# Kernel optimization log

Hardware: AMD Instinct MI355X
Metric: run time of the kernel (lower is better)

## Reference

```python
import jax, jax.numpy as jnp
import numpy as np

B, N, C, IC = 8, 4096, 1024, 256
EPS = 1e-5


def setup_inputs() -> dict:
    key = jax.random.key(0)
    ks = jax.random.split(key, 10)
    s = 0.02  # keep activations well-scaled
    return {
        "v": jax.random.normal(ks[0], (B, N, C), jnp.float32),
        "g_w": jax.random.normal(ks[1], (IC, C), jnp.float32) * s,
        "g_b": jax.random.normal(ks[2], (IC,), jnp.float32) * s,
        "theta_w": jax.random.normal(ks[3], (IC, C), jnp.float32) * s,
        "theta_b": jax.random.normal(ks[4], (IC,), jnp.float32) * s,
        "phi_w": jax.random.normal(ks[5], (IC, C), jnp.float32) * s,
        "phi_b": jax.random.normal(ks[6], (IC,), jnp.float32) * s,
        "W_w": jax.random.normal(ks[7], (C, IC), jnp.float32) * s,
        "W_b": jax.random.normal(ks[8], (C,), jnp.float32) * s,
        "bn_gamma": jnp.ones((C,), jnp.float32),
        "bn_beta": jnp.zeros((C,), jnp.float32),
    }


def reference(v, g_w, g_b, theta_w, theta_b, phi_w, phi_b, W_w, W_b, bn_gamma, bn_beta):
    # v: (B, N, C). All Conv1d(k=1) == per-token matmul.
    g_v = jnp.einsum("bnc,ic->bni", v, g_w) + g_b          # (B, N, IC)
    theta_v = jnp.einsum("bnc,ic->bni", v, theta_w) + theta_b
    phi_v = jnp.einsum("bnc,ic->bni", v, phi_w) + phi_b
    n = v.shape[1]
    # Affinity: R = theta @ phi^T, normalized by N (no softmax)
    R = jnp.einsum("bni,bmi->bnm", theta_v, phi_v) / n      # (B, N, N)
    y = jnp.einsum("bnm,bmi->bni", R, g_v)                  # (B, N, IC)
    W_y = jnp.einsum("bni,ci->bnc", y, W_w) + W_b           # (B, N, C)
    # BatchNorm1d training mode: per-channel stats over (B, N), biased var
    mean = jnp.mean(W_y, axis=(0, 1))
    var = jnp.var(W_y, axis=(0, 1))
    W_y = (W_y - mean) * jax.lax.rsqrt(var + EPS) * bn_gamma + bn_beta
    return W_y + v                                          # residual, (B, N, C)
```

## Files before the change

### kernel.cpp

```cpp
#include <hip/hip_runtime.h>
#include <hip/hip_bf16.h>
#include <stdint.h>


using bf16 = __hip_bfloat16;
typedef __attribute__((ext_vector_type(8))) short short8;
typedef __attribute__((ext_vector_type(4))) float f32x4;
typedef __attribute__((ext_vector_type(4))) short short4v;

#define DEVI static __device__ __forceinline__

DEVI float bf2f(unsigned short u) {
  union { unsigned int i; float f; } x; x.i = ((unsigned int)u) << 16; return x.f;
}
DEVI unsigned short f2bf(float f) {
  __hip_bfloat16 h = __float2bfloat16(f);
  return *reinterpret_cast<unsigned short*>(&h);
}

DEVI void gld16(const void* g, void* l) {
  __builtin_amdgcn_global_load_lds((__attribute__((address_space(1))) void*)g,
                                   (__attribute__((address_space(3))) void*)l,
                                   16, 0, 0);
}

DEVI void mfma_loop(const bf16* A, int ldA, const bf16* B, int ldB,
                    int kiters, bf16* lds_a, bf16* lds_b, f32x4 acc[4][4])
{
  const int tid = threadIdx.x;
  const int lane = tid & 63;
  const int w = tid >> 6;
  const int wr = w >> 1, wc = w & 1;
  const int srow = w * 32 + (lane >> 2);
  const int scol = (lane & 3) * 8;
  const bf16* ga0 = A + (size_t)srow * ldA + scol;
  const bf16* ga1 = A + (size_t)(srow + 16) * ldA + scol;
  const bf16* gb0 = B + (size_t)srow * ldB + scol;
  const bf16* gb1 = B + (size_t)(srow + 16) * ldB + scol;
  bf16* la0 = lds_a + w * 1024 + lane * 8;
  bf16* la1 = la0 + 512;
  bf16* lb0 = lds_b + w * 1024 + lane * 8;
  bf16* lb1 = lb0 + 512;
  const int frow = lane & 15;
  const int fk = (lane >> 4) * 8;
  const bf16* ra = lds_a + (wr * 64 + frow) * 32 + fk;
  const bf16* rb = lds_b + (wc * 64 + frow) * 32 + fk;
  for (int it = 0; it < kiters; ++it) {
    gld16(ga0, la0); gld16(ga1, la1);
    gld16(gb0, lb0); gld16(gb1, lb1);
    ga0 += 32; ga1 += 32; gb0 += 32; gb1 += 32;
    __syncthreads();
    short8 af[4], bfr[4];
#pragma unroll
    for (int i = 0; i < 4; ++i) af[i] = *(const short8*)(ra + i * 512);
#pragma unroll
    for (int j = 0; j < 4; ++j) bfr[j] = *(const short8*)(rb + j * 512);
#pragma unroll
    for (int i = 0; i < 4; ++i)
#pragma unroll
      for (int j = 0; j < 4; ++j)
        acc[i][j] = __builtin_amdgcn_mfma_f32_16x16x32_bf16(af[i], bfr[j], acc[i][j], 0, 0, 0);
    __syncthreads();
  }
}

#define ACC_INIT(acc)                                   \
  _Pragma("unroll") for (int i = 0; i < 4; ++i)         \
  _Pragma("unroll") for (int j = 0; j < 4; ++j)         \
      acc[i][j] = (f32x4){0.f, 0.f, 0.f, 0.f};

__global__ __launch_bounds__(256) void k_cast(const float* __restrict__ in, bf16* __restrict__ out)
{
  const size_t idx = ((size_t)blockIdx.x * 256 + threadIdx.x) * 8;
  float4 a = *(const float4*)(in + idx);
  float4 b = *(const float4*)(in + idx + 4);
  short8 o;
  o[0] = (short)f2bf(a.x); o[1] = (short)f2bf(a.y);
  o[2] = (short)f2bf(a.z); o[3] = (short)f2bf(a.w);
  o[4] = (short)f2bf(b.x); o[5] = (short)f2bf(b.y);
  o[6] = (short)f2bf(b.z); o[7] = (short)f2bf(b.w);
  *(short8*)(out + idx) = o;
}

__global__ __launch_bounds__(256) void k_proj(
    const bf16* __restrict__ vbf,
    const bf16* __restrict__ w_th, const float* __restrict__ b_th,
    const bf16* __restrict__ w_ph, const float* __restrict__ b_ph,
    const bf16* __restrict__ w_g,  const float* __restrict__ b_g,
    bf16* __restrict__ theta, bf16* __restrict__ phiT, bf16* __restrict__ gT)
{
  __shared__ __align__(16) char smem[34048];
  bf16* lds_a = (bf16*)smem;
  bf16* lds_b = (bf16*)(smem + 8192);
  unsigned short* lds_t = (unsigned short*)smem;

  const int tt = blockIdx.x;
  const int yy = blockIdx.y;
  const int proj = yy >> 1;
  const int icb = (yy & 1) * 128;
  const bf16* wsel = (proj == 0) ? w_th : ((proj == 1) ? w_ph : w_g);
  const float* bsel = (proj == 0) ? b_th : ((proj == 1) ? b_ph : b_g);

  const size_t t0 = (size_t)tt * 128;
  f32x4 acc[4][4];
  ACC_INIT(acc);
  mfma_loop(vbf + t0 * 1024, 1024, wsel + (size_t)icb * 1024, 1024, 32, lds_a, lds_b, acc);

  const int tid = threadIdx.x, lane = tid & 63, w = tid >> 6;
  const int wr = w >> 1, wc = w & 1, quad = lane >> 4, l15 = lane & 15;
  float biasv[4];
#pragma unroll
  for (int j = 0; j < 4; ++j) biasv[j] = bsel[icb + wc * 64 + j * 16 + l15];

  if (proj == 0) {
#pragma unroll
    for (int i = 0; i < 4; ++i)
#pragma unroll
      for (int j = 0; j < 4; ++j)
#pragma unroll
        for (int r = 0; r < 4; ++r) {
          int m = wr * 64 + i * 16 + quad * 4 + r;
          int n = wc * 64 + j * 16 + l15;
          theta[(t0 + m) * 256 + icb + n] = __float2bfloat16(acc[i][j][r] + biasv[j]);
        }
  } else {
#pragma unroll
    for (int i = 0; i < 4; ++i)
#pragma unroll
      for (int j = 0; j < 4; ++j)
#pragma unroll
        for (int r = 0; r < 4; ++r) {
          int m = wr * 64 + i * 16 + quad * 4 + r;
          int n = wc * 64 + j * 16 + l15;
          lds_t[m * 133 + n] = f2bf(acc[i][j][r] + biasv[j]);
        }
    __syncthreads();
    bf16* outT = (proj == 1) ? phiT : gT;
    const int bb = (int)(t0 >> 12);
    const int n0 = (int)(t0 & 4095);
    const int tg = tid & 7;
    const int ch0 = tid >> 3;
#pragma unroll
    for (int half = 0; half < 2; ++half)
#pragma unroll
      for (int cc = 0; cc < 4; ++cc) {
        int ch = ch0 + cc * 32;
        int tok0 = half * 64 + tg * 8;
        short8 pk;
#pragma unroll
        for (int r = 0; r < 8; ++r) pk[r] = (short)lds_t[(tok0 + r) * 133 + ch];
        *(short8*)(outT + ((size_t)(bb * 256 + icb + ch)) * 4096 + n0 + tok0) = pk;
      }
  }
}

__global__ __launch_bounds__(256) void k_affin(
    const bf16* __restrict__ phiT, const bf16* __restrict__ gT, float* __restrict__ M)
{
  __shared__ __align__(16) char smem[16384];
  bf16* lds_a = (bf16*)smem;
  bf16* lds_b = (bf16*)(smem + 8192);
  const int kc = blockIdx.x;
  const int jt = blockIdx.y >> 1;
  const int it2 = blockIdx.y & 1;
  const int bb = blockIdx.z;
  f32x4 acc[4][4];
  ACC_INIT(acc);
  const bf16* A = phiT + ((size_t)bb * 256 + jt * 128) * 4096 + kc * 512;
  const bf16* B = gT   + ((size_t)bb * 256 + it2 * 128) * 4096 + kc * 512;
  mfma_loop(A, 4096, B, 4096, 16, lds_a, lds_b, acc);
  const int tid = threadIdx.x, lane = tid & 63, w = tid >> 6;
  const int wr = w >> 1, wc = w & 1, quad = lane >> 4, l15 = lane & 15;
  float* Mb = M + (size_t)bb * 65536;
#pragma unroll
  for (int i = 0; i < 4; ++i)
#pragma unroll
    for (int j = 0; j < 4; ++j)
#pragma unroll
      for (int r = 0; r < 4; ++r) {
        int m = wr * 64 + i * 16 + quad * 4 + r;
        int n = wc * 64 + j * 16 + l15;
        atomicAdd(&Mb[(size_t)(jt * 128 + m) * 256 + it2 * 128 + n], acc[i][j][r]);
      }
}

__global__ __launch_bounds__(256) void k_mconv(const float* __restrict__ M, bf16* __restrict__ Mbf)
{
  int i = blockIdx.x * 256 + threadIdx.x;
  Mbf[i] = __float2bfloat16(M[i] * (1.0f / 4096.0f));
}

__global__ __launch_bounds__(256) void k_pt(
    const bf16* __restrict__ Ww, const bf16* __restrict__ Mbf, bf16* __restrict__ PT)
{
  __shared__ __align__(16) char smem[16384];
  bf16* lds_a = (bf16*)smem;
  bf16* lds_b = (bf16*)(smem + 8192);
  const int ct = blockIdx.x;
  const int jt = blockIdx.y;
  const int bb = blockIdx.z;
  f32x4 acc[4][4];
  ACC_INIT(acc);
  mfma_loop(Ww + (size_t)ct * 128 * 256, 256,
            Mbf + ((size_t)bb * 256 + jt * 128) * 256, 256, 8, lds_a, lds_b, acc);
  const int tid = threadIdx.x, lane = tid & 63, w = tid >> 6;
  const int wr = w >> 1, wc = w & 1, quad = lane >> 4, l15 = lane & 15;
#pragma unroll
  for (int i = 0; i < 4; ++i)
#pragma unroll
    for (int j = 0; j < 4; ++j)
#pragma unroll
      for (int r = 0; r < 4; ++r) {
        int m = wr * 64 + i * 16 + quad * 4 + r;
        int n = wc * 64 + j * 16 + l15;
        PT[((size_t)bb * 1024 + ct * 128 + m) * 256 + jt * 128 + n] = __float2bfloat16(acc[i][j][r]);
      }
}

__global__ __launch_bounds__(256) void k_wy(
    const bf16* __restrict__ theta, const bf16* __restrict__ PT, bf16* __restrict__ Wy)
{
  __shared__ __align__(16) char smem[16384];
  bf16* lds_a = (bf16*)smem;
  bf16* lds_b = (bf16*)(smem + 8192);
  const size_t t0 = (size_t)blockIdx.x * 128;
  const int ct = blockIdx.y;
  const int bb = (int)(t0 >> 12);
  f32x4 acc[4][4];
  ACC_INIT(acc);
  mfma_loop(theta + t0 * 256, 256,
            PT + ((size_t)bb * 1024 + ct * 128) * 256, 256, 8, lds_a, lds_b, acc);
  const int tid = threadIdx.x, lane = tid & 63, w = tid >> 6;
  const int wr = w >> 1, wc = w & 1, quad = lane >> 4, l15 = lane & 15;
#pragma unroll
  for (int i = 0; i < 4; ++i)
#pragma unroll
    for (int j = 0; j < 4; ++j)
#pragma unroll
      for (int r = 0; r < 4; ++r) {
        int m = wr * 64 + i * 16 + quad * 4 + r;
        int n = wc * 64 + j * 16 + l15;
        Wy[(t0 + m) * 1024 + ct * 128 + n] = __float2bfloat16(acc[i][j][r]);
      }
}

__global__ __launch_bounds__(256) void k_stats(const bf16* __restrict__ Wy,
                                               float* __restrict__ sums, float* __restrict__ sumsq)
{
  const int t0 = blockIdx.x * 128;
  const int c0 = threadIdx.x * 4;
  float s[4] = {0.f, 0.f, 0.f, 0.f}, q[4] = {0.f, 0.f, 0.f, 0.f};
  for (int r = 0; r < 128; ++r) {
    short4v u = *(const short4v*)(Wy + (size_t)(t0 + r) * 1024 + c0);
#pragma unroll
    for (int k = 0; k < 4; ++k) {
      float f = bf2f((unsigned short)u[k]);
      s[k] += f; q[k] += f * f;
    }
  }
#pragma unroll
  for (int k = 0; k < 4; ++k) {
    atomicAdd(&sums[c0 + k], s[k]);
    atomicAdd(&sumsq[c0 + k], q[k]);
  }
}

__global__ void k_norm(const float* __restrict__ sums, const float* __restrict__ sumsq,
                       const float* __restrict__ gamma, const float* __restrict__ beta,
                       float* __restrict__ scale, float* __restrict__ shift)
{
  int c = blockIdx.x * 256 + threadIdx.x;
  float mean = sums[c] * (1.0f / 32768.0f);
  float var = sumsq[c] * (1.0f / 32768.0f) - mean * mean;
  float sc = gamma[c] * rsqrtf(var + 1e-5f);
  scale[c] = sc;
  shift[c] = beta[c] - mean * sc;
}

__global__ __launch_bounds__(256) void k_out(const bf16* __restrict__ Wy, const float* __restrict__ v,
                                             const float* __restrict__ scale, const float* __restrict__ shift,
                                             float* __restrict__ out)
{
  const size_t idx = ((size_t)blockIdx.x * 256 + threadIdx.x) * 4;
  const int c = (int)(idx & 1023);
  short4v wv = *(const short4v*)(Wy + idx);
  float4 vv = *(const float4*)(v + idx);
  float4 o;
  o.x = bf2f((unsigned short)wv[0]) * scale[c + 0] + shift[c + 0] + vv.x;
  o.y = bf2f((unsigned short)wv[1]) * scale[c + 1] + shift[c + 1] + vv.y;
  o.z = bf2f((unsigned short)wv[2]) * scale[c + 2] + shift[c + 2] + vv.z;
  o.w = bf2f((unsigned short)wv[3]) * scale[c + 3] + shift[c + 3] + vv.w;
  *(float4*)(out + idx) = o;
}

extern "C" void kernel_launch(void* const* d_in, const int* in_sizes, int n_in,
                              void* d_out, int out_size, void* d_ws, size_t ws_size,
                              hipStream_t stream)
{
  (void)in_sizes; (void)n_in; (void)out_size; (void)ws_size;
  const float* v    = (const float*)d_in[0];
  const float* g_w  = (const float*)d_in[1];
  const float* g_b  = (const float*)d_in[2];
  const float* th_w = (const float*)d_in[3];
  const float* th_b = (const float*)d_in[4];
  const float* ph_w = (const float*)d_in[5];
  const float* ph_b = (const float*)d_in[6];
  const float* W_w  = (const float*)d_in[7];
  const float* gamma = (const float*)d_in[9];
  const float* beta  = (const float*)d_in[10];
  float* out = (float*)d_out;

  char* ws = (char*)d_ws;
  bf16* vbf  = (bf16*)ws;
  bf16* Wy   = (bf16*)ws;
  ws += (size_t)32768 * 1024 * 2;
  bf16* theta = (bf16*)ws;  ws += (size_t)32768 * 256 * 2;
  bf16* phiT  = (bf16*)ws;  ws += (size_t)32768 * 256 * 2;
  bf16* gT    = (bf16*)ws;  ws += (size_t)32768 * 256 * 2;
  float* M    = (float*)ws; ws += (size_t)8 * 65536 * 4;
  bf16* Mbf   = (bf16*)ws;  ws += (size_t)8 * 65536 * 2;
  bf16* PT    = (bf16*)ws;  ws += (size_t)8 * 1024 * 256 * 2;
  bf16* thwb  = (bf16*)ws;  ws += (size_t)256 * 1024 * 2;
  bf16* phwb  = (bf16*)ws;  ws += (size_t)256 * 1024 * 2;
  bf16* gwb   = (bf16*)ws;  ws += (size_t)256 * 1024 * 2;
  bf16* Wwb   = (bf16*)ws;  ws += (size_t)1024 * 256 * 2;
  float* sums = (float*)ws; ws += 4096;
  float* sumsq= (float*)ws; ws += 4096;
  float* scale= (float*)ws; ws += 4096;
  float* shift= (float*)ws; ws += 4096;

  hipMemsetAsync(M, 0, (size_t)8 * 65536 * 4, stream);
  hipMemsetAsync(sums, 0, 8192, stream);

  k_cast <<<16384, 256, 0, stream>>>(v, vbf);
  k_cast <<<128, 256, 0, stream>>>(th_w, thwb);
  k_cast <<<128, 256, 0, stream>>>(ph_w, phwb);
  k_cast <<<128, 256, 0, stream>>>(g_w, gwb);
  k_cast <<<128, 256, 0, stream>>>(W_w, Wwb);

  k_proj <<<dim3(256, 6), 256, 0, stream>>>(vbf, thwb, th_b, phwb, ph_b, gwb, g_b, theta, phiT, gT);
  k_affin<<<dim3(8, 4, 8), 256, 0, stream>>>(phiT, gT, M);
  k_mconv<<<2048, 256, 0, stream>>>(M, Mbf);
  k_pt   <<<dim3(8, 2, 8), 256, 0, stream>>>(Wwb, Mbf, PT);
  k_wy   <<<dim3(256, 8), 256, 0, stream>>>(theta, PT, Wy);
  k_stats<<<256, 256, 0, stream>>>(Wy, sums, sumsq);
  k_norm <<<4, 256, 0, stream>>>(sums, sumsq, gamma, beta, scale, shift);
  k_out  <<<32768, 256, 0, stream>>>(Wy, v, scale, shift, out);
}
```

Before: 470.7 us.

## Fuse v cast into projection GEMM and BN stats into Wy epilogue

```diff
diff --git a/kernel.cpp b/kernel.cpp
--- a/kernel.cpp
+++ b/kernel.cpp
@@ -22,6 +22,15 @@
   __builtin_amdgcn_global_load_lds((__attribute__((address_space(1))) void*)g,
                                    (__attribute__((address_space(3))) void*)l,
                                    16, 0, 0);
+}
+
+DEVI short8 cvt8(float4 a, float4 b) {
+  short8 o;
+  o[0] = (short)f2bf(a.x); o[1] = (short)f2bf(a.y);
+  o[2] = (short)f2bf(a.z); o[3] = (short)f2bf(a.w);
+  o[4] = (short)f2bf(b.x); o[5] = (short)f2bf(b.y);
+  o[6] = (short)f2bf(b.z); o[7] = (short)f2bf(b.w);
+  return o;
 }
 
 DEVI void mfma_loop(const bf16* A, int ldA, const bf16* B, int ldB,
@@ -64,26 +73,77 @@
   }
 }
 
+DEVI void mfma_loop_f32a(const float* A, int ldA, const bf16* B, int ldB,
+                         int kiters, bf16* lds_a, bf16* lds_b, f32x4 acc[4][4])
+{
+  const int tid = threadIdx.x;
+  const int lane = tid & 63;
+  const int w = tid >> 6;
+  const int wr = w >> 1, wc = w & 1;
+  const int srow = w * 32 + (lane >> 2);
+  const int scol = (lane & 3) * 8;
+  const float* ga0 = A + (size_t)srow * ldA + scol;
+  const float* ga1 = A + (size_t)(srow + 16) * ldA + scol;
+  const bf16* gb0 = B + (size_t)srow * ldB + scol;
+  const bf16* gb1 = B + (size_t)(srow + 16) * ldB + scol;
+  bf16* la0 = lds_a + w * 1024 + lane * 8;
+  bf16* la1 = la0 + 512;
+  bf16* lb0 = lds_b + w * 1024 + lane * 8;
+  bf16* lb1 = lb0 + 512;
+  const int frow = lane & 15;
+  const int fk = (lane >> 4) * 8;
+  const bf16* ra = lds_a + (wr * 64 + frow) * 32 + fk;
+  const bf16* rb = lds_b + (wc * 64 + frow) * 32 + fk;
+  for (int it = 0; it < kiters; ++it) {
+    gld16(gb0, lb0); gld16(gb1, lb1);
+    float4 a00 = *(const float4*)ga0;
+    float4 a01 = *(const float4*)(ga0 + 4);
+    float4 a10 = *(const float4*)ga1;
+    float4 a11 = *(const float4*)(ga1 + 4);
+    *(short8*)la0 = cvt8(a00, a01);
+    *(short8*)la1 = cvt8(a10, a11);
+    ga0 += 32; ga1 += 32; gb0 += 32; gb1 += 32;
+    __syncthreads();
+    short8 af[4], bfr[4];
+#pragma unroll
+    for (int i = 0; i < 4; ++i) af[i] = *(const short8*)(ra + i * 512);
+#pragma unroll
+    for (int j = 0; j < 4; ++j) bfr[j] = *(const short8*)(rb + j * 512);
+#pragma unroll
+    for (int i = 0; i < 4; ++i)
+#pragma unroll
+      for (int j = 0; j < 4; ++j)
+        acc[i][j] = __builtin_amdgcn_mfma_f32_16x16x32_bf16(af[i], bfr[j], acc[i][j], 0, 0, 0);
+    __syncthreads();
+  }
+}
+
 #define ACC_INIT(acc)                                   \
   _Pragma("unroll") for (int i = 0; i < 4; ++i)         \
   _Pragma("unroll") for (int j = 0; j < 4; ++j)         \
       acc[i][j] = (f32x4){0.f, 0.f, 0.f, 0.f};
 
-__global__ __launch_bounds__(256) void k_cast(const float* __restrict__ in, bf16* __restrict__ out)
-{
+__global__ __launch_bounds__(256) void k_castw(
+    const float* __restrict__ s0, const float* __restrict__ s1,
+    const float* __restrict__ s2, const float* __restrict__ s3,
+    bf16* __restrict__ d0, bf16* __restrict__ d1,
+    bf16* __restrict__ d2, bf16* __restrict__ d3)
+{
+  const float* in; bf16* out;
+  switch (blockIdx.y) {
+    case 0:  in = s0; out = d0; break;
+    case 1:  in = s1; out = d1; break;
+    case 2:  in = s2; out = d2; break;
+    default: in = s3; out = d3; break;
+  }
   const size_t idx = ((size_t)blockIdx.x * 256 + threadIdx.x) * 8;
   float4 a = *(const float4*)(in + idx);
   float4 b = *(const float4*)(in + idx + 4);
-  short8 o;
-  o[0] = (short)f2bf(a.x); o[1] = (short)f2bf(a.y);
-  o[2] = (short)f2bf(a.z); o[3] = (short)f2bf(a.w);
-  o[4] = (short)f2bf(b.x); o[5] = (short)f2bf(b.y);
-  o[6] = (short)f2bf(b.z); o[7] = (short)f2bf(b.w);
-  *(short8*)(out + idx) = o;
+  *(short8*)(out + idx) = cvt8(a, b);
 }
 
 __global__ __launch_bounds__(256) void k_proj(
-    const bf16* __restrict__ vbf,
+    const float* __restrict__ v,
     const bf16* __restrict__ w_th, const float* __restrict__ b_th,
     const bf16* __restrict__ w_ph, const float* __restrict__ b_ph,
     const bf16* __restrict__ w_g,  const float* __restrict__ b_g,
@@ -104,7 +164,7 @@
   const size_t t0 = (size_t)tt * 128;
   f32x4 acc[4][4];
   ACC_INIT(acc);
-  mfma_loop(vbf + t0 * 1024, 1024, wsel + (size_t)icb * 1024, 1024, 32, lds_a, lds_b, acc);
+  mfma_loop_f32a(v + t0 * 1024, 1024, wsel + (size_t)icb * 1024, 1024, 32, lds_a, lds_b, acc);
 
   const int tid = threadIdx.x, lane = tid & 63, w = tid >> 6;
   const int wr = w >> 1, wc = w & 1, quad = lane >> 4, l15 = lane & 15;
@@ -218,7 +278,8 @@
 }
 
 __global__ __launch_bounds__(256) void k_wy(
-    const bf16* __restrict__ theta, const bf16* __restrict__ PT, bf16* __restrict__ Wy)
+    const bf16* __restrict__ theta, const bf16* __restrict__ PT, bf16* __restrict__ Wy,
+    float* __restrict__ sums, float* __restrict__ sumsq)
 {
   __shared__ __align__(16) char smem[16384];
   bf16* lds_a = (bf16*)smem;
@@ -232,6 +293,7 @@
             PT + ((size_t)bb * 1024 + ct * 128) * 256, 256, 8, lds_a, lds_b, acc);
   const int tid = threadIdx.x, lane = tid & 63, w = tid >> 6;
   const int wr = w >> 1, wc = w & 1, quad = lane >> 4, l15 = lane & 15;
+  float ps[4] = {0.f, 0.f, 0.f, 0.f}, pq[4] = {0.f, 0.f, 0.f, 0.f};
 #pragma unroll
   for (int i = 0; i < 4; ++i)
 #pragma unroll
@@ -240,28 +302,22 @@
       for (int r = 0; r < 4; ++r) {
         int m = wr * 64 + i * 16 + quad * 4 + r;
         int n = wc * 64 + j * 16 + l15;
-        Wy[(t0 + m) * 1024 + ct * 128 + n] = __float2bfloat16(acc[i][j][r]);
+        float f = acc[i][j][r];
+        Wy[(t0 + m) * 1024 + ct * 128 + n] = __float2bfloat16(f);
+        ps[j] += f; pq[j] += f * f;
       }
-}
-
-__global__ __launch_bounds__(256) void k_stats(const bf16* __restrict__ Wy,
-                                               float* __restrict__ sums, float* __restrict__ sumsq)
-{
-  const int t0 = blockIdx.x * 128;
-  const int c0 = threadIdx.x * 4;
-  float s[4] = {0.f, 0.f, 0.f, 0.f}, q[4] = {0.f, 0.f, 0.f, 0.f};
-  for (int r = 0; r < 128; ++r) {
-    short4v u = *(const short4v*)(Wy + (size_t)(t0 + r) * 1024 + c0);
-#pragma unroll
-    for (int k = 0; k < 4; ++k) {
-      float f = bf2f((unsigned short)u[k]);
-      s[k] += f; q[k] += f * f;
+#pragma unroll
+  for (int j = 0; j < 4; ++j) {
+    ps[j] += __shfl_xor(ps[j], 16); ps[j] += __shfl_xor(ps[j], 32);
+    pq[j] += __shfl_xor(pq[j], 16); pq[j] += __shfl_xor(pq[j], 32);
+  }
+  if (quad == 0) {
+#pragma unroll
+    for (int j = 0; j < 4; ++j) {
+      int c = ct * 128 + wc * 64 + j * 16 + l15;
+      atomicAdd(&sums[c], ps[j]);
+      atomicAdd(&sumsq[c], pq[j]);
     }
-  }
-#pragma unroll
-  for (int k = 0; k < 4; ++k) {
-    atomicAdd(&sums[c0 + k], s[k]);
-    atomicAdd(&sumsq[c0 + k], q[k]);
   }
 }
 
@@ -311,7 +367,6 @@
   float* out = (float*)d_out;
 
   char* ws = (char*)d_ws;
-  bf16* vbf  = (bf16*)ws;
   bf16* Wy   = (bf16*)ws;
   ws += (size_t)32768 * 1024 * 2;
   bf16* theta = (bf16*)ws;  ws += (size_t)32768 * 256 * 2;
@@ -332,18 +387,13 @@
   hipMemsetAsync(M, 0, (size_t)8 * 65536 * 4, stream);
   hipMemsetAsync(sums, 0, 8192, stream);
 
-  k_cast <<<16384, 256, 0, stream>>>(v, vbf);
-  k_cast <<<128, 256, 0, stream>>>(th_w, thwb);
-  k_cast <<<128, 256, 0, stream>>>(ph_w, phwb);
-  k_cast <<<128, 256, 0, stream>>>(g_w, gwb);
-  k_cast <<<128, 256, 0, stream>>>(W_w, Wwb);
-
-  k_proj <<<dim3(256, 6), 256, 0, stream>>>(vbf, thwb, th_b, phwb, ph_b, gwb, g_b, theta, phiT, gT);
+  k_castw<<<dim3(128, 4), 256, 0, stream>>>(th_w, ph_w, g_w, W_w, thwb, phwb, gwb, Wwb);
+
+  k_proj <<<dim3(256, 6), 256, 0, stream>>>(v, thwb, th_b, phwb, ph_b, gwb, g_b, theta, phiT, gT);
   k_affin<<<dim3(8, 4, 8), 256, 0, stream>>>(phiT, gT, M);
   k_mconv<<<2048, 256, 0, stream>>>(M, Mbf);
   k_pt   <<<dim3(8, 2, 8), 256, 0, stream>>>(Wwb, Mbf, PT);
-  k_wy   <<<dim3(256, 8), 256, 0, stream>>>(theta, PT, Wy);
-  k_stats<<<256, 256, 0, stream>>>(Wy, sums, sumsq);
+  k_wy   <<<dim3(256, 8), 256, 0, stream>>>(theta, PT, Wy, sums, sumsq);
   k_norm <<<4, 256, 0, stream>>>(sums, sumsq, gamma, beta, scale, shift);
   k_out  <<<32768, 256, 0, stream>>>(Wy, v, scale, shift, out);
 }
```

Measured after the change: 470.0 us. Within noise of the previous version (-0.2%).

## Fuse BN statistics into Wy GEMM epilogue and merge cast launches

Applied to the files above, without the earlier changes.

```diff
diff --git a/kernel.cpp b/kernel.cpp
--- a/kernel.cpp
+++ b/kernel.cpp
@@ -22,6 +22,15 @@
   __builtin_amdgcn_global_load_lds((__attribute__((address_space(1))) void*)g,
                                    (__attribute__((address_space(3))) void*)l,
                                    16, 0, 0);
+}
+
+DEVI short8 cvt8(float4 a, float4 b) {
+  short8 o;
+  o[0] = (short)f2bf(a.x); o[1] = (short)f2bf(a.y);
+  o[2] = (short)f2bf(a.z); o[3] = (short)f2bf(a.w);
+  o[4] = (short)f2bf(b.x); o[5] = (short)f2bf(b.y);
+  o[6] = (short)f2bf(b.z); o[7] = (short)f2bf(b.w);
+  return o;
 }
 
 DEVI void mfma_loop(const bf16* A, int ldA, const bf16* B, int ldB,
@@ -69,17 +78,31 @@
   _Pragma("unroll") for (int j = 0; j < 4; ++j)         \
       acc[i][j] = (f32x4){0.f, 0.f, 0.f, 0.f};
 
-__global__ __launch_bounds__(256) void k_cast(const float* __restrict__ in, bf16* __restrict__ out)
-{
-  const size_t idx = ((size_t)blockIdx.x * 256 + threadIdx.x) * 8;
+__global__ __launch_bounds__(256) void k_cast_all(
+    const float* __restrict__ v, bf16* __restrict__ vbf,
+    const float* __restrict__ s0, const float* __restrict__ s1,
+    const float* __restrict__ s2, const float* __restrict__ s3,
+    bf16* __restrict__ d0, bf16* __restrict__ d1,
+    bf16* __restrict__ d2, bf16* __restrict__ d3)
+{
+  const float* in; bf16* out; size_t base;
+  const int bx = blockIdx.x;
+  if (bx < 16384) {
+    in = v; out = vbf; base = (size_t)bx * 2048;
+  } else {
+    const int wq = bx - 16384;
+    switch (wq >> 7) {
+      case 0:  in = s0; out = d0; break;
+      case 1:  in = s1; out = d1; break;
+      case 2:  in = s2; out = d2; break;
+      default: in = s3; out = d3; break;
+    }
+    base = (size_t)(wq & 127) * 2048;
+  }
+  const size_t idx = base + (size_t)threadIdx.x * 8;
   float4 a = *(const float4*)(in + idx);
   float4 b = *(const float4*)(in + idx + 4);
-  short8 o;
-  o[0] = (short)f2bf(a.x); o[1] = (short)f2bf(a.y);
-  o[2] = (short)f2bf(a.z); o[3] = (short)f2bf(a.w);
-  o[4] = (short)f2bf(b.x); o[5] = (short)f2bf(b.y);
-  o[6] = (short)f2bf(b.z); o[7] = (short)f2bf(b.w);
-  *(short8*)(out + idx) = o;
+  *(short8*)(out + idx) = cvt8(a, b);
 }
 
 __global__ __launch_bounds__(256) void k_proj(
@@ -218,7 +241,8 @@
 }
 
 __global__ __launch_bounds__(256) void k_wy(
-    const bf16* __restrict__ theta, const bf16* __restrict__ PT, bf16* __restrict__ Wy)
+    const bf16* __restrict__ theta, const bf16* __restrict__ PT, bf16* __restrict__ Wy,
+    float* __restrict__ sums, float* __restrict__ sumsq)
 {
   __shared__ __align__(16) char smem[16384];
   bf16* lds_a = (bf16*)smem;
@@ -232,6 +256,7 @@
             PT + ((size_t)bb * 1024 + ct * 128) * 256, 256, 8, lds_a, lds_b, acc);
   const int tid = threadIdx.x, lane = tid & 63, w = tid >> 6;
   const int wr = w >> 1, wc = w & 1, quad = lane >> 4, l15 = lane & 15;
+  float ps[4] = {0.f, 0.f, 0.f, 0.f}, pq[4] = {0.f, 0.f, 0.f, 0.f};
 #pragma unroll
   for (int i = 0; i < 4; ++i)
 #pragma unroll
@@ -240,56 +265,48 @@
       for (int r = 0; r < 4; ++r) {
         int m = wr * 64 + i * 16 + quad * 4 + r;
         int n = wc * 64 + j * 16 + l15;
-        Wy[(t0 + m) * 1024 + ct * 128 + n] = __float2bfloat16(acc[i][j][r]);
+        float f = acc[i][j][r];
+        Wy[(t0 + m) * 1024 + ct * 128 + n] = __float2bfloat16(f);
+        ps[j] += f; pq[j] += f * f;
       }
-}
-
-__global__ __launch_bounds__(256) void k_stats(const bf16* __restrict__ Wy,
-                                               float* __restrict__ sums, float* __restrict__ sumsq)
-{
-  const int t0 = blockIdx.x * 128;
-  const int c0 = threadIdx.x * 4;
-  float s[4] = {0.f, 0.f, 0.f, 0.f}, q[4] = {0.f, 0.f, 0.f, 0.f};
-  for (int r = 0; r < 128; ++r) {
-    short4v u = *(const short4v*)(Wy + (size_t)(t0 + r) * 1024 + c0);
-#pragma unroll
-    for (int k = 0; k < 4; ++k) {
-      float f = bf2f((unsigned short)u[k]);
-      s[k] += f; q[k] += f * f;
+#pragma unroll
+  for (int j = 0; j < 4; ++j) {
+    ps[j] += __shfl_xor(ps[j], 16); ps[j] += __shfl_xor(ps[j], 32);
+    pq[j] += __shfl_xor(pq[j], 16); pq[j] += __shfl_xor(pq[j], 32);
+  }
+  if (quad == 0) {
+#pragma unroll
+    for (int j = 0; j < 4; ++j) {
+      int c = ct * 128 + wc * 64 + j * 16 + l15;
+      atomicAdd(&sums[c], ps[j]);
+      atomicAdd(&sumsq[c], pq[j]);
     }
   }
-#pragma unroll
-  for (int k = 0; k < 4; ++k) {
-    atomicAdd(&sums[c0 + k], s[k]);
-    atomicAdd(&sumsq[c0 + k], q[k]);
-  }
-}
-
-__global__ void k_norm(const float* __restrict__ sums, const float* __restrict__ sumsq,
-                       const float* __restrict__ gamma, const float* __restrict__ beta,
-                       float* __restrict__ scale, float* __restrict__ shift)
-{
-  int c = blockIdx.x * 256 + threadIdx.x;
-  float mean = sums[c] * (1.0f / 32768.0f);
-  float var = sumsq[c] * (1.0f / 32768.0f) - mean * mean;
-  float sc = gamma[c] * rsqrtf(var + 1e-5f);
-  scale[c] = sc;
-  shift[c] = beta[c] - mean * sc;
 }
 
 __global__ __launch_bounds__(256) void k_out(const bf16* __restrict__ Wy, const float* __restrict__ v,
-                                             const float* __restrict__ scale, const float* __restrict__ shift,
+                                             const float* __restrict__ sums, const float* __restrict__ sumsq,
+                                             const float* __restrict__ gamma, const float* __restrict__ beta,
                                              float* __restrict__ out)
 {
   const size_t idx = ((size_t)blockIdx.x * 256 + threadIdx.x) * 4;
   const int c = (int)(idx & 1023);
+  float4 sm = *(const float4*)(sums + c);
+  float4 sq = *(const float4*)(sumsq + c);
+  float4 gm = *(const float4*)(gamma + c);
+  float4 bt = *(const float4*)(beta + c);
   short4v wv = *(const short4v*)(Wy + idx);
   float4 vv = *(const float4*)(v + idx);
   float4 o;
-  o.x = bf2f((unsigned short)wv[0]) * scale[c + 0] + shift[c + 0] + vv.x;
-  o.y = bf2f((unsigned short)wv[1]) * scale[c + 1] + shift[c + 1] + vv.y;
-  o.z = bf2f((unsigned short)wv[2]) * scale[c + 2] + shift[c + 2] + vv.z;
-  o.w = bf2f((unsigned short)wv[3]) * scale[c + 3] + shift[c + 3] + vv.w;
+#pragma unroll
+  for (int k = 0; k < 4; ++k) {
+    float smk = (&sm.x)[k], sqk = (&sq.x)[k], gmk = (&gm.x)[k], btk = (&bt.x)[k];
+    float mean = smk * (1.0f / 32768.0f);
+    float var = sqk * (1.0f / 32768.0f) - mean * mean;
+    float sc = gmk * rsqrtf(var + 1e-5f);
+    float sh = btk - mean * sc;
+    (&o.x)[k] = bf2f((unsigned short)wv[k]) * sc + sh + (&vv.x)[k];
+  }
   *(float4*)(out + idx) = o;
 }
 
@@ -326,24 +343,17 @@
   bf16* Wwb   = (bf16*)ws;  ws += (size_t)1024 * 256 * 2;
   float* sums = (float*)ws; ws += 4096;
   float* sumsq= (float*)ws; ws += 4096;
-  float* scale= (float*)ws; ws += 4096;
-  float* shift= (float*)ws; ws += 4096;
 
   hipMemsetAsync(M, 0, (size_t)8 * 65536 * 4, stream);
   hipMemsetAsync(sums, 0, 8192, stream);
 
-  k_cast <<<16384, 256, 0, stream>>>(v, vbf);
-  k_cast <<<128, 256, 0, stream>>>(th_w, thwb);
-  k_cast <<<128, 256, 0, stream>>>(ph_w, phwb);
-  k_cast <<<128, 256, 0, stream>>>(g_w, gwb);
-  k_cast <<<128, 256, 0, stream>>>(W_w, Wwb);
+  k_cast_all<<<16384 + 512, 256, 0, stream>>>(v, vbf, th_w, ph_w, g_w, W_w,
+                                              thwb, phwb, gwb, Wwb);
 
   k_proj <<<dim3(256, 6), 256, 0, stream>>>(vbf, thwb, th_b, phwb, ph_b, gwb, g_b, theta, phiT, gT);
   k_affin<<<dim3(8, 4, 8), 256, 0, stream>>>(phiT, gT, M);
   k_mconv<<<2048, 256, 0, stream>>>(M, Mbf);
   k_pt   <<<dim3(8, 2, 8), 256, 0, stream>>>(Wwb, Mbf, PT);
-  k_wy   <<<dim3(256, 8), 256, 0, stream>>>(theta, PT, Wy);
-  k_stats<<<256, 256, 0, stream>>>(Wy, sums, sumsq);
-  k_norm <<<4, 256, 0, stream>>>(sums, sumsq, gamma, beta, scale, shift);
-  k_out  <<<32768, 256, 0, stream>>>(Wy, v, scale, shift, out);
-}
+  k_wy   <<<dim3(256, 8), 256, 0, stream>>>(theta, PT, Wy, sums, sumsq);
+  k_out  <<<32768, 256, 0, stream>>>(Wy, v, sums, sumsq, gamma, beta, out);
+}
```

Result: no change. 471.2 us (+0.1%).
